# Optimization experiments

Measured on AMD Instinct MI355X. Metric: run time of the kernel, lower is better.

The kernel has to match this reference:

```python
import jax, jax.numpy as jnp
import numpy as np

L, B, T, V, E, H = 6, 4, 1024, 32000, 768, 12
D = E // H  # head_size = 64


def setup_inputs() -> dict:
    key = jax.random.key(0)
    ks = jax.random.split(key, 12)
    s = 0.02
    n = lambda k, shape: jax.random.normal(k, shape, jnp.float32) * s
    return {
        "idx": jax.random.randint(ks[0], (B, T), 0, V),
        "tok_emb": n(ks[1], (V, E)),
        "pos_emb": n(ks[2], (T, E)),
        "ln1_w": jnp.ones((L, E)), "ln1_b": jnp.zeros((L, E)),
        "wq": n(ks[3], (L, E, H, D)),
        "wk": n(ks[4], (L, E, H, D)),
        "wv": n(ks[5], (L, E, H, D)),
        "wo": n(ks[6], (L, E, E)), "bo": jnp.zeros((L, E)),
        "ln2_w": jnp.ones((L, E)), "ln2_b": jnp.zeros((L, E)),
        "w1": n(ks[7], (L, E, 4 * E)), "b1": jnp.zeros((L, 4 * E)),
        "w2": n(ks[8], (L, 4 * E, E)), "b2": jnp.zeros((L, E)),
        "lnf_w": jnp.ones((E,)), "lnf_b": jnp.zeros((E,)),
        "head_w": n(ks[9], (E, V)), "head_b": jnp.zeros((V,)),
    }


def _ln(x, w, b, eps=1e-5):
    m = x.mean(-1, keepdims=True)
    v = ((x - m) ** 2).mean(-1, keepdims=True)
    return (x - m) * jax.lax.rsqrt(v + eps) * w + b


def _forward(idx, tok_emb, pos_emb, ln1_w, ln1_b, wq, wk, wv, wo, bo,
             ln2_w, ln2_b, w1, b1, w2, b2, lnf_w, lnf_b, head_w, head_b):
    t = idx.shape[1]
    x = tok_emb[idx] + pos_emb[None, :t]          # [B,T,E]
    causal = jnp.tril(jnp.ones((t, t), bool))     # tril buffer
    scale = jnp.asarray(D, x.dtype) ** -0.5       # k.shape[-1] ** -0.5

    def block(x, p):
        l1w, l1b, Wq, Wk, Wv, Wo, Bo, l2w, l2b, W1, B1, W2, B2 = p
        h = _ln(x, l1w, l1b)
        q = jnp.einsum('btc,chd->bthd', h, Wq)
        k = jnp.einsum('btc,chd->bthd', h, Wk)
        v = jnp.einsum('btc,chd->bthd', h, Wv)
        wei = jnp.einsum('bqhd,bkhd->bhqk', q, k) * scale
        wei = jnp.where(causal, wei, -jnp.inf)
        wei = jax.nn.softmax(wei, axis=-1)
        att = jnp.einsum('bhqk,bkhd->bqhd', wei, v).reshape(x.shape)
        x = x + (att @ Wo + Bo)
        h2 = _ln(x, l2w, l2b)
        x = x + (jax.nn.relu(h2 @ W1 + B1) @ W2 + B2)
        return x, None

    params = (ln1_w, ln1_b, wq, wk, wv, wo, bo, ln2_w, ln2_b, w1, b1, w2, b2)
    x, _ = jax.lax.scan(block, x, params)
    x = _ln(x, lnf_w, lnf_b)
    return x @ head_w + head_b                    # [B,T,V] logits


def reference(idx, tok_emb, pos_emb, ln1_w, ln1_b, wq, wk, wv, wo, bo,
              ln2_w, ln2_b, w1, b1, w2, b2, lnf_w, lnf_b, head_w, head_b):
    return _forward(idx, tok_emb, pos_emb, ln1_w, ln1_b, wq, wk, wv, wo, bo,
                    ln2_w, ln2_b, w1, b1, w2, b2, lnf_w, lnf_b, head_w, head_b)
```

## Files before the change

kernel.cpp:

```cpp
#include <hip/hip_runtime.h>
#include <hip/hip_bf16.h>
#include <math.h>

#define L_LAYERS 6
#define BB 4
#define TT 1024
#define VV 32000
#define EE 768
#define HH 12
#define DD 64
#define BT (BB * TT)

typedef unsigned short u16;
typedef unsigned int   u32;
typedef __attribute__((ext_vector_type(8))) short short8;
typedef __attribute__((ext_vector_type(8))) unsigned short ushort8v;
typedef __attribute__((ext_vector_type(4))) unsigned short ushort4v;
typedef __attribute__((ext_vector_type(4))) float f32x4;

__device__ __forceinline__ float b2f_lo(u32 u) { union { u32 i; float f; } c; c.i = u << 16;          return c.f; }
__device__ __forceinline__ float b2f_hi(u32 u) { union { u32 i; float f; } c; c.i = u & 0xffff0000u;  return c.f; }
__device__ __forceinline__ u16  f2b(float f)   { union { float f; u32 i; } c{f}; u32 r = c.i + 0x7fffu + ((c.i >> 16) & 1u); return (u16)(r >> 16); }

__device__ __forceinline__ void gload16(const void* g, void* l) {
    __builtin_amdgcn_global_load_lds(
        (const __attribute__((address_space(1))) void*)g,
        (__attribute__((address_space(3))) void*)l, 16, 0, 0);
}

__global__ __launch_bounds__(256) void embed_kernel(
    const int* __restrict__ idx, const float* __restrict__ tok_emb,
    const float* __restrict__ pos_emb, float* __restrict__ x)
{
    int i = blockIdx.x * 256 + threadIdx.x;
    int e  = i % EE;
    int bt = i / EE;
    int t  = bt % TT;
    int tok = idx[bt];
    x[i] = tok_emb[(size_t)tok * EE + e] + pos_emb[(size_t)t * EE + e];
}

__global__ __launch_bounds__(256) void ln_kernel(
    const float* __restrict__ X, const float* __restrict__ w,
    const float* __restrict__ b, u16* __restrict__ Y)
{
    const int lane = threadIdx.x & 63;
    const size_t row = blockIdx.x * 4 + (threadIdx.x >> 6);
    const float* x = X + row * EE;

    f32x4 v[3];
    #pragma unroll
    for (int k = 0; k < 3; k++)
        v[k] = *(const f32x4*)&x[lane * 4 + k * 256];

    float s = 0.0f;
    #pragma unroll
    for (int k = 0; k < 3; k++) s += v[k][0] + v[k][1] + v[k][2] + v[k][3];
    #pragma unroll
    for (int off = 32; off; off >>= 1) s += __shfl_xor(s, off);
    const float mean = s * (1.0f / EE);

    float q = 0.0f;
    #pragma unroll
    for (int k = 0; k < 3; k++)
        #pragma unroll
        for (int j = 0; j < 4; j++) {
            v[k][j] -= mean;
            q += v[k][j] * v[k][j];
        }
    #pragma unroll
    for (int off = 32; off; off >>= 1) q += __shfl_xor(q, off);
    const float rstd = rsqrtf(q * (1.0f / EE) + 1e-5f);

    u16* y = Y + row * EE;
    #pragma unroll
    for (int k = 0; k < 3; k++) {
        const f32x4 wv = *(const f32x4*)&w[lane * 4 + k * 256];
        const f32x4 bv = *(const f32x4*)&b[lane * 4 + k * 256];
        ushort4v o;
        #pragma unroll
        for (int j = 0; j < 4; j++) o[j] = f2b(v[k][j] * rstd * wv[j] + bv[j]);
        *(ushort4v*)&y[lane * 4 + k * 256] = o;
    }
}

__device__ __forceinline__ void transpose_tile(
    const float* __restrict__ W, u16* __restrict__ Wt,
    int K, int N, int kt, int nt)
{
    __shared__ float t[32][33];
    const int k0 = kt * 32;
    const int n0 = nt * 32;
    const int c = threadIdx.x & 31;
    const int r = threadIdx.x >> 5;
    #pragma unroll
    for (int i = 0; i < 4; i++)
        t[r + i * 8][c] = W[(size_t)(k0 + r + i * 8) * N + n0 + c];
    __syncthreads();
    #pragma unroll
    for (int i = 0; i < 4; i++) {
        int rr = r + i * 8;
        Wt[(size_t)(n0 + rr) * K + k0 + c] = f2b(t[c][rr]);
    }
}

__global__ __launch_bounds__(256) void transpose_cvt(
    const float* __restrict__ W, u16* __restrict__ Wt, int K, int N)
{
    transpose_tile(W, Wt, K, N, blockIdx.y, blockIdx.x);
}

__global__ __launch_bounds__(256) void transpose_layer(
    const float* __restrict__ wq, const float* __restrict__ wk,
    const float* __restrict__ wv, const float* __restrict__ wo,
    const float* __restrict__ w1, const float* __restrict__ w2,
    u16* __restrict__ wt)
{
    const int t = blockIdx.x;
    if (t < 2304) {
        const int m = t / 576, r = t % 576;
        const float* Ws[4] = {wq, wk, wv, wo};
        transpose_tile(Ws[m], wt + (size_t)m * 768 * 768, 768, 768, r / 24, r % 24);
    } else if (t < 4608) {
        const int r = t - 2304;
        transpose_tile(w1, wt + (size_t)4 * 768 * 768, 768, 3072, r / 96, r % 96);
    } else {
        const int r = t - 4608;
        transpose_tile(w2, wt + (size_t)4 * 768 * 768 + (size_t)3072 * 768,
                       3072, 768, r / 24, r % 24);
    }
}

template<int RELU, int RES, int OUTBF, int MFRAG>
__global__ __launch_bounds__(256) void gemm_bf16(
    const u16* __restrict__ A, const u16* __restrict__ Bt,
    const float* __restrict__ bias, const float* __restrict__ res,
    void* __restrict__ Cv, int M, int N, int K)
{
    constexpr int TM = MFRAG * 32;
    __shared__ u16 As[TM * 64];
    __shared__ u16 Bs[128 * 64];

    const int tid  = threadIdx.x;
    const int lane = tid & 63;
    const int w    = tid >> 6;
    const int wr   = w >> 1, wc = w & 1;

    const int gx  = gridDim.x;
    const int nwg = gx * gridDim.y;
    const int lin = blockIdx.y * gx + blockIdx.x;
    const int q8  = nwg >> 3;
    const int s   = (lin & 7) * q8 + (lin >> 3);
    const int m0  = (s % gx) * TM;
    const int n0  = (s / gx) * 128;

    const int cs = (lane & 7) ^ (lane >> 3);
    const int rl = lane >> 3;

    int aoff[2 * MFRAG], boff[8];
    const int kq = lane >> 4;
    #pragma unroll
    for (int mi = 0; mi < MFRAG; mi++) {
        int rg = wr * (MFRAG * 16) + mi * 16 + (lane & 15);
        #pragma unroll
        for (int ks = 0; ks < 2; ks++)
            aoff[2 * mi + ks] = rg * 64 + (((ks * 4 + kq) ^ (rg & 7)) * 8);
    }
    #pragma unroll
    for (int ni = 0; ni < 4; ni++) {
        int rg = wc * 64 + ni * 16 + (lane & 15);
        #pragma unroll
        for (int ks = 0; ks < 2; ks++)
            boff[2 * ni + ks] = rg * 64 + (((ks * 4 + kq) ^ (rg & 7)) * 8);
    }

    f32x4 acc[MFRAG][4] = {};

    for (int k0 = 0; k0 < K; k0 += 64) {
        __syncthreads();
        #pragma unroll
        for (int i = 0; i < MFRAG; i++) {
            const int seg = i * 4 + w;
            const int row = seg * 8 + rl;
            gload16(A + (size_t)(m0 + row) * K + k0 + cs * 8, &As[seg * 512]);
        }
        #pragma unroll
        for (int i = 0; i < 4; i++) {
            const int seg = i * 4 + w;
            const int row = seg * 8 + rl;
            gload16(Bt + (size_t)(n0 + row) * K + k0 + cs * 8, &Bs[seg * 512]);
        }
        __syncthreads();
        #pragma unroll
        for (int ks = 0; ks < 2; ks++) {
            short8 af[MFRAG], bfv[4];
            #pragma unroll
            for (int mi = 0; mi < MFRAG; mi++) af[mi] = *(const short8*)&As[aoff[2 * mi + ks]];
            #pragma unroll
            for (int ni = 0; ni < 4; ni++) bfv[ni] = *(const short8*)&Bs[boff[2 * ni + ks]];
            #pragma unroll
            for (int mi = 0; mi < MFRAG; mi++)
                #pragma unroll
                for (int ni = 0; ni < 4; ni++)
                    acc[mi][ni] = __builtin_amdgcn_mfma_f32_16x16x32_bf16(
                        af[mi], bfv[ni], acc[mi][ni], 0, 0, 0);
        }
    }

    const int rbase = m0 + wr * (MFRAG * 16) + (lane >> 4) * 4;
    const int cbase = n0 + wc * 64 + (lane & 15);
    #pragma unroll
    for (int ni = 0; ni < 4; ni++) {
        const int c = cbase + ni * 16;
        const float bv = bias ? bias[c] : 0.0f;
        #pragma unroll
        for (int mi = 0; mi < MFRAG; mi++) {
            const int r = rbase + mi * 16;
            #pragma unroll
            for (int i = 0; i < 4; i++) {
                float v = acc[mi][ni][i] + bv;
                const size_t off = (size_t)(r + i) * N + c;
                if (RES)  v += res[off];
                if (RELU) v = fmaxf(v, 0.0f);
                if (OUTBF) ((u16*)Cv)[off] = f2b(v);
                else       ((float*)Cv)[off] = v;
            }
        }
    }
}

#define AST 72
__global__ __launch_bounds__(256) void attn_mfma(
    const u16* __restrict__ qkv, u16* __restrict__ O)
{
    const int tid = threadIdx.x;
    const int qi = blockIdx.x;
    const int h  = blockIdx.y;
    const int b  = blockIdx.z;
    const int q0 = qi * 64;

    __shared__ u16 Ks[2][64 * 64];
    __shared__ u16 Vt[2][64 * AST];
    __shared__ u16 Ps[64 * AST];

    const int lane = tid & 63;
    const int w    = tid >> 6;
    const int lr   = lane & 15;
    const int lk   = lane >> 4;

    const int cs = (lane & 7) ^ (lane >> 3);
    const int rl = lane >> 3;
    const int vk2 = tid & 31;
    const int vdc = tid >> 5;

    {
        const int sr = tid >> 2, sc = tid & 3;
        const u16* src = qkv + (size_t)(b * TT + q0 + sr) * 2304 + h * 64 + sc * 16;
        *(ushort8v*)&Ps[sr * AST + sc * 16]     = *(const ushort8v*)src;
        *(ushort8v*)&Ps[sr * AST + sc * 16 + 8] = *(const ushort8v*)(src + 8);
    }
    __syncthreads();
    short8 aq[2];
    #pragma unroll
    for (int ks = 0; ks < 2; ks++)
        aq[ks] = *(const short8*)&Ps[(w * 16 + lr) * AST + lk * 8 + ks * 32];

    ushort8v vr0, vr1;
    auto K_ISSUE = [&](int t, int bf) {
        const int k0 = t * 64;
        #pragma unroll
        for (int j = 0; j < 2; ++j) {
            const int seg = j * 4 + w;
            const int row = seg * 8 + rl;
            gload16(qkv + (size_t)(b * TT + k0 + row) * 2304 + 768 + h * 64 + cs * 8,
                    &Ks[bf][seg * 512]);
        }
    };
    auto V_LOAD = [&](int t) {
        const int k0 = t * 64;
        const u16* p = qkv + (size_t)(b * TT + k0 + 2 * vk2) * 2304 + 1536 + h * 64 + vdc * 8;
        vr0 = *(const ushort8v*)p;
        vr1 = *(const ushort8v*)(p + 2304);
    };
    auto V_WRITE = [&](int bf) {
        #pragma unroll
        for (int j = 0; j < 8; ++j) {
            const u32 val = (u32)vr0[j] | ((u32)vr1[j] << 16);
            *(u32*)&Vt[bf][(vdc * 8 + j) * AST + 2 * vk2] = val;
        }
    };

    K_ISSUE(0, 0);
    V_LOAD(0);
    V_WRITE(0);
    __syncthreads();

    f32x4 oacc[4] = {};
    float m_run[4], l_run[4];
    #pragma unroll
    for (int i = 0; i < 4; i++) { m_run[i] = -3.0e38f; l_run[i] = 0.0f; }

    const int qrow = q0 + w * 16 + lk * 4;
    const float SC = 0.18033688f;

    for (int t = 0; t <= qi; ++t) {
        const int cur = t & 1;

        f32x4 sfrag[4] = {};
        #pragma unroll
        for (int ks = 0; ks < 2; ks++)
            #pragma unroll
            for (int nt = 0; nt < 4; nt++) {
                const int rg = nt * 16 + lr;
                short8 bk = *(const short8*)&Ks[cur][rg * 64 + (((ks * 4 + lk) ^ (rg & 7)) * 8)];
                sfrag[nt] = __builtin_amdgcn_mfma_f32_16x16x32_bf16(aq[ks], bk, sfrag[nt], 0, 0, 0);
            }

        if (t < qi) { K_ISSUE(t + 1, cur ^ 1); V_LOAD(t + 1); }

        const int k0 = t * 64;
        float sv[4][4], mxv[4];
        float need = 0.0f;
        #pragma unroll
        for (int i = 0; i < 4; i++) {
            float mx = -3.0e38f;
            #pragma unroll
            for (int nt = 0; nt < 4; nt++) {
                float s = sfrag[nt][i] * SC;
                if (t == qi && (k0 + nt * 16 + lr) > (qrow + i)) s = -3.0e38f;
                sv[i][nt] = s;
                mx = fmaxf(mx, s);
            }
            mx = fmaxf(mx, __shfl_xor(mx, 1));
            mx = fmaxf(mx, __shfl_xor(mx, 2));
            mx = fmaxf(mx, __shfl_xor(mx, 4));
            mx = fmaxf(mx, __shfl_xor(mx, 8));
            mxv[i] = mx;
            need = fmaxf(need, mx - m_run[i]);
        }
        if (!__all(need <= 11.5f)) {
            #pragma unroll
            for (int i = 0; i < 4; i++) {
                const float m_new = fmaxf(m_run[i], mxv[i]);
                const float scale = exp2f(m_run[i] - m_new);
                l_run[i] *= scale;
                #pragma unroll
                for (int dt = 0; dt < 4; dt++) oacc[dt][i] *= scale;
                m_run[i] = m_new;
            }
        }
        #pragma unroll
        for (int i = 0; i < 4; i++) {
            float rs = 0.0f;
            #pragma unroll
            for (int nt = 0; nt < 4; nt++) {
                const float p = exp2f(sv[i][nt] - m_run[i]);
                sv[i][nt] = p;
                rs += p;
            }
            rs += __shfl_xor(rs, 1);
            rs += __shfl_xor(rs, 2);
            rs += __shfl_xor(rs, 4);
            rs += __shfl_xor(rs, 8);
            l_run[i] += rs;
        }

        #pragma unroll
        for (int i = 0; i < 4; i++)
            #pragma unroll
            for (int nt = 0; nt < 4; nt++)
                Ps[(w * 16 + lk * 4 + i) * AST + nt * 16 + lr] = f2b(sv[i][nt]);

        #pragma unroll
        for (int ks = 0; ks < 2; ks++) {
            short8 ap = *(const short8*)&Ps[(w * 16 + lr) * AST + lk * 8 + ks * 32];
            #pragma unroll
            for (int dt = 0; dt < 4; dt++) {
                short8 bv = *(const short8*)&Vt[cur][(dt * 16 + lr) * AST + lk * 8 + ks * 32];
                oacc[dt] = __builtin_amdgcn_mfma_f32_16x16x32_bf16(ap, bv, oacc[dt], 0, 0, 0);
            }
        }

        if (t < qi) V_WRITE(cur ^ 1);
        __syncthreads();
    }

    #pragma unroll
    for (int i = 0; i < 4; i++) {
        const float inv = 1.0f / l_run[i];
        u16* dst = O + (size_t)(b * TT + q0 + w * 16 + lk * 4 + i) * 768 + h * 64 + lr;
        #pragma unroll
        for (int dt = 0; dt < 4; dt++)
            dst[dt * 16] = f2b(oacc[dt][i] * inv);
    }
}

extern "C" void kernel_launch(void* const* d_in, const int* in_sizes, int n_in,
                              void* d_out, int out_size, void* d_ws, size_t ws_size,
                              hipStream_t stream)
{
    (void)in_sizes; (void)n_in; (void)out_size; (void)ws_size;

    const int*   idx     = (const int*)  d_in[0];
    const float* tok_emb = (const float*)d_in[1];
    const float* pos_emb = (const float*)d_in[2];
    const float* ln1_w   = (const float*)d_in[3];
    const float* ln1_b   = (const float*)d_in[4];
    const float* wq      = (const float*)d_in[5];
    const float* wk      = (const float*)d_in[6];
    const float* wv      = (const float*)d_in[7];
    const float* wo      = (const float*)d_in[8];
    const float* bo      = (const float*)d_in[9];
    const float* ln2_w   = (const float*)d_in[10];
    const float* ln2_b   = (const float*)d_in[11];
    const float* w1      = (const float*)d_in[12];
    const float* b1      = (const float*)d_in[13];
    const float* w2      = (const float*)d_in[14];
    const float* b2      = (const float*)d_in[15];
    const float* lnf_w   = (const float*)d_in[16];
    const float* lnf_b   = (const float*)d_in[17];
    const float* head_w  = (const float*)d_in[18];
    const float* head_b  = (const float*)d_in[19];
    float* out = (float*)d_out;

    const size_t S = (size_t)BT * EE;
    float* x   = (float*)d_ws;
    u16*  qkv  = (u16*)(x + S);
    u16*  hb   = qkv + (size_t)BT * 2304;
    u16*  ffh  = hb + S;
    u16*  wt   = ffh + (size_t)BT * 3072;

    embed_kernel<<<BT * EE / 256, 256, 0, stream>>>(idx, tok_emb, pos_emb, x);

    for (int l = 0; l < L_LAYERS; l++) {
        const size_t oE  = (size_t)l * EE;
        const size_t oEE = (size_t)l * EE * EE;
        const size_t oEF = (size_t)l * EE * 4 * EE;

        transpose_layer<<<6912, 256, 0, stream>>>(
            wq + oEE, wk + oEE, wv + oEE, wo + oEE, w1 + oEF, w2 + oEF, wt);

        ln_kernel<<<BT / 4, 256, 0, stream>>>(x, ln1_w + oE, ln1_b + oE, hb);
        gemm_bf16<0, 0, 1, 4><<<dim3(BT / 128, 2304 / 128), 256, 0, stream>>>(
            hb, wt, nullptr, nullptr, qkv, BT, 2304, 768);
        attn_mfma<<<dim3(TT / 64, HH, BB), 256, 0, stream>>>(qkv, hb);
        gemm_bf16<0, 1, 0, 2><<<dim3(BT / 64, 768 / 128), 256, 0, stream>>>(
            hb, wt + (size_t)3 * 768 * 768, bo + oE, x, x, BT, 768, 768);
        ln_kernel<<<BT / 4, 256, 0, stream>>>(x, ln2_w + oE, ln2_b + oE, hb);
        gemm_bf16<1, 0, 1, 4><<<dim3(BT / 128, 3072 / 128), 256, 0, stream>>>(
            hb, wt + (size_t)4 * 768 * 768, b1 + (size_t)l * 4 * EE, nullptr, ffh, BT, 3072, 768);
        gemm_bf16<0, 1, 0, 2><<<dim3(BT / 64, 768 / 128), 256, 0, stream>>>(
            ffh, wt + (size_t)4 * 768 * 768 + (size_t)3072 * 768, b2 + oE, x, x, BT, 768, 3072);
    }

    ln_kernel<<<BT / 4, 256, 0, stream>>>(x, lnf_w, lnf_b, hb);
    transpose_cvt<<<dim3(VV / 32, EE / 32), 256, 0, stream>>>(head_w, wt, EE, VV);
    gemm_bf16<0, 0, 0, 4><<<dim3(BT / 128, VV / 128), 256, 0, stream>>>(
        hb, wt, head_b, nullptr, out, BT, VV, 768);
}
```

Measured before the change: 1.555 ms.

## Enlarge attention query tile to 128 rows with 8 waves; drop GEMM tile swizzle

The attention kernel now processes 128 query rows per block with 512 threads, so each K/V tile loaded into shared memory serves twice as many queries. Waves whose rows lie entirely before a key tile skip its compute, and the causal mask is applied only on diagonal tiles. This cuts global K/V traffic per query and halves the number of blocks, at the cost of fewer, larger blocks and some idle waves near the diagonal. Separately, the GEMM drops its block-index swizzle and uses a plain row/column mapping, which may change L2 locality.

```diff
diff --git a/kernel.cpp b/kernel.cpp
--- a/kernel.cpp
+++ b/kernel.cpp
@@ -145,14 +145,8 @@
     const int lane = tid & 63;
     const int w    = tid >> 6;
     const int wr   = w >> 1, wc = w & 1;
-
-    const int gx  = gridDim.x;
-    const int nwg = gx * gridDim.y;
-    const int lin = blockIdx.y * gx + blockIdx.x;
-    const int q8  = nwg >> 3;
-    const int s   = (lin & 7) * q8 + (lin >> 3);
-    const int m0  = (s % gx) * TM;
-    const int n0  = (s / gx) * 128;
+    const int m0 = blockIdx.x * TM;
+    const int n0 = blockIdx.y * 128;
 
     const int cs = (lane & 7) ^ (lane >> 3);
     const int rl = lane >> 3;
@@ -230,18 +224,18 @@
 }
 
 #define AST 72
-__global__ __launch_bounds__(256) void attn_mfma(
+__global__ __launch_bounds__(512) void attn_mfma(
     const u16* __restrict__ qkv, u16* __restrict__ O)
 {
     const int tid = threadIdx.x;
     const int qi = blockIdx.x;
     const int h  = blockIdx.y;
     const int b  = blockIdx.z;
-    const int q0 = qi * 64;
+    const int q0 = qi * 128;
 
     __shared__ u16 Ks[2][64 * 64];
     __shared__ u16 Vt[2][64 * AST];
-    __shared__ u16 Ps[64 * AST];
+    __shared__ u16 Ps[128 * AST];
 
     const int lane = tid & 63;
     const int w    = tid >> 6;
@@ -251,7 +245,7 @@
     const int cs = (lane & 7) ^ (lane >> 3);
     const int rl = lane >> 3;
     const int vk2 = tid & 31;
-    const int vdc = tid >> 5;
+    const int vdc = (tid >> 5) & 15;
 
     {
         const int sr = tid >> 2, sc = tid & 3;
@@ -265,28 +259,24 @@
     for (int ks = 0; ks < 2; ks++)
         aq[ks] = *(const short8*)&Ps[(w * 16 + lr) * AST + lk * 8 + ks * 32];
 
-    ushort8v vr0, vr1;
+    ushort4v vr0, vr1;
     auto K_ISSUE = [&](int t, int bf) {
         const int k0 = t * 64;
-        #pragma unroll
-        for (int j = 0; j < 2; ++j) {
-            const int seg = j * 4 + w;
-            const int row = seg * 8 + rl;
-            gload16(qkv + (size_t)(b * TT + k0 + row) * 2304 + 768 + h * 64 + cs * 8,
-                    &Ks[bf][seg * 512]);
-        }
+        const int row = w * 8 + rl;
+        gload16(qkv + (size_t)(b * TT + k0 + row) * 2304 + 768 + h * 64 + cs * 8,
+                &Ks[bf][w * 512]);
     };
     auto V_LOAD = [&](int t) {
         const int k0 = t * 64;
-        const u16* p = qkv + (size_t)(b * TT + k0 + 2 * vk2) * 2304 + 1536 + h * 64 + vdc * 8;
-        vr0 = *(const ushort8v*)p;
-        vr1 = *(const ushort8v*)(p + 2304);
+        const u16* p = qkv + (size_t)(b * TT + k0 + 2 * vk2) * 2304 + 1536 + h * 64 + vdc * 4;
+        vr0 = *(const ushort4v*)p;
+        vr1 = *(const ushort4v*)(p + 2304);
     };
     auto V_WRITE = [&](int bf) {
         #pragma unroll
-        for (int j = 0; j < 8; ++j) {
+        for (int j = 0; j < 4; ++j) {
             const u32 val = (u32)vr0[j] | ((u32)vr1[j] << 16);
-            *(u32*)&Vt[bf][(vdc * 8 + j) * AST + 2 * vk2] = val;
+            *(u32*)&Vt[bf][(vdc * 4 + j) * AST + 2 * vk2] = val;
         }
     };
 
@@ -301,87 +291,95 @@
     for (int i = 0; i < 4; i++) { m_run[i] = -3.0e38f; l_run[i] = 0.0f; }
 
     const int qrow = q0 + w * 16 + lk * 4;
+    const int wmax = q0 + w * 16 + 15;
+    const int ntile = 2 * qi + 2;
     const float SC = 0.18033688f;
 
-    for (int t = 0; t <= qi; ++t) {
+    for (int t = 0; t < ntile; ++t) {
         const int cur = t & 1;
+        const int k0 = t * 64;
+        const bool active = (k0 <= wmax);
 
         f32x4 sfrag[4] = {};
-        #pragma unroll
-        for (int ks = 0; ks < 2; ks++)
-            #pragma unroll
-            for (int nt = 0; nt < 4; nt++) {
-                const int rg = nt * 16 + lr;
-                short8 bk = *(const short8*)&Ks[cur][rg * 64 + (((ks * 4 + lk) ^ (rg & 7)) * 8)];
-                sfrag[nt] = __builtin_amdgcn_mfma_f32_16x16x32_bf16(aq[ks], bk, sfrag[nt], 0, 0, 0);
+        if (active) {
+            #pragma unroll
+            for (int ks = 0; ks < 2; ks++)
+                #pragma unroll
+                for (int nt = 0; nt < 4; nt++) {
+                    const int rg = nt * 16 + lr;
+                    short8 bk = *(const short8*)&Ks[cur][rg * 64 + (((ks * 4 + lk) ^ (rg & 7)) * 8)];
+                    sfrag[nt] = __builtin_amdgcn_mfma_f32_16x16x32_bf16(aq[ks], bk, sfrag[nt], 0, 0, 0);
+                }
+        }
+
+        if (t + 1 < ntile) { K_ISSUE(t + 1, cur ^ 1); V_LOAD(t + 1); }
+
+        if (active) {
+            const bool diag = (k0 + 63 > qrow);
+            float sv[4][4], mxv[4];
+            float need = 0.0f;
+            #pragma unroll
+            for (int i = 0; i < 4; i++) {
+                float mx = -3.0e38f;
+                #pragma unroll
+                for (int nt = 0; nt < 4; nt++) {
+                    float s = sfrag[nt][i] * SC;
+                    if (diag && (k0 + nt * 16 + lr) > (qrow + i)) s = -3.0e38f;
+                    sv[i][nt] = s;
+                    mx = fmaxf(mx, s);
+                }
+                mx = fmaxf(mx, __shfl_xor(mx, 1));
+                mx = fmaxf(mx, __shfl_xor(mx, 2));
+                mx = fmaxf(mx, __shfl_xor(mx, 4));
+                mx = fmaxf(mx, __shfl_xor(mx, 8));
+                mxv[i] = mx;
+                need = fmaxf(need, mx - m_run[i]);
             }
-
-        if (t < qi) { K_ISSUE(t + 1, cur ^ 1); V_LOAD(t + 1); }
-
-        const int k0 = t * 64;
-        float sv[4][4], mxv[4];
-        float need = 0.0f;
-        #pragma unroll
-        for (int i = 0; i < 4; i++) {
-            float mx = -3.0e38f;
-            #pragma unroll
-            for (int nt = 0; nt < 4; nt++) {
-                float s = sfrag[nt][i] * SC;
-                if (t == qi && (k0 + nt * 16 + lr) > (qrow + i)) s = -3.0e38f;
-                sv[i][nt] = s;
-                mx = fmaxf(mx, s);
+            if (!__all(need <= 11.5f)) {
+                #pragma unroll
+                for (int i = 0; i < 4; i++) {
+                    const float m_new = fmaxf(m_run[i], mxv[i]);
+                    const float scale = exp2f(m_run[i] - m_new);
+                    l_run[i] *= scale;
+                    #pragma unroll
+                    for (int dt = 0; dt < 4; dt++) oacc[dt][i] *= scale;
+                    m_run[i] = m_new;
+                }
             }
-            mx = fmaxf(mx, __shfl_xor(mx, 1));
-            mx = fmaxf(mx, __shfl_xor(mx, 2));
-            mx = fmaxf(mx, __shfl_xor(mx, 4));
-            mx = fmaxf(mx, __shfl_xor(mx, 8));
-            mxv[i] = mx;
-            need = fmaxf(need, mx - m_run[i]);
-        }
-        if (!__all(need <= 11.5f)) {
             #pragma unroll
             for (int i = 0; i < 4; i++) {
-                const float m_new = fmaxf(m_run[i], mxv[i]);
-                const float scale = exp2f(m_run[i] - m_new);
-                l_run[i] *= scale;
-                #pragma unroll
-                for (int dt = 0; dt < 4; dt++) oacc[dt][i] *= scale;
-                m_run[i] = m_new;
+                float rs = 0.0f;
+                #pragma unroll
+                for (int nt = 0; nt < 4; nt++) {
+                    const float p = exp2f(sv[i][nt] - m_run[i]);
+                    sv[i][nt] = p;
+                    rs += p;
+                }
+                rs += __shfl_xor(rs, 1);
+                rs += __shfl_xor(rs, 2);
+                rs += __shfl_xor(rs, 4);
+                rs += __shfl_xor(rs, 8);
+                l_run[i] += rs;
             }
-        }
-        #pragma unroll
-        for (int i = 0; i < 4; i++) {
-            float rs = 0.0f;
-            #pragma unroll
-            for (int nt = 0; nt < 4; nt++) {
-                const float p = exp2f(sv[i][nt] - m_run[i]);
-                sv[i][nt] = p;
-                rs += p;
+
+            #pragma unroll
+            for (int i = 0; i < 4; i++)
+                #pragma unroll
+                for (int nt = 0; nt < 4; nt++)
+                    Ps[(w * 16 + lk * 4 + i) * AST + nt * 16 + lr] = f2b(sv[i][nt]);
+
+            #pragma unroll
+            for (int ks = 0; ks < 2; ks++) {
+                short8 ap = *(const short8*)&Ps[(w * 16 + lr) * AST + lk * 8 + ks * 32];
+                #pragma unroll
+                for (int dt = 0; dt < 4; dt++) {
+                    short8 bv = *(const short8*)&Vt[cur][(dt * 16 + lr) * AST + lk * 8 + ks * 32];
+                    oacc[dt] = __builtin_amdgcn_mfma_f32_16x16x32_bf16(ap, bv, oacc[dt], 0, 0, 0);
+                }
             }
-            rs += __shfl_xor(rs, 1);
-            rs += __shfl_xor(rs, 2);
-            rs += __shfl_xor(rs, 4);
-            rs += __shfl_xor(rs, 8);
-            l_run[i] += rs;
-        }
-
-        #pragma unroll
-        for (int i = 0; i < 4; i++)
-            #pragma unroll
-            for (int nt = 0; nt < 4; nt++)
-                Ps[(w * 16 + lk * 4 + i) * AST + nt * 16 + lr] = f2b(sv[i][nt]);
-
-        #pragma unroll
-        for (int ks = 0; ks < 2; ks++) {
-            short8 ap = *(const short8*)&Ps[(w * 16 + lr) * AST + lk * 8 + ks * 32];
-            #pragma unroll
-            for (int dt = 0; dt < 4; dt++) {
-                short8 bv = *(const short8*)&Vt[cur][(dt * 16 + lr) * AST + lk * 8 + ks * 32];
-                oacc[dt] = __builtin_amdgcn_mfma_f32_16x16x32_bf16(ap, bv, oacc[dt], 0, 0, 0);
-            }
-        }
-
-        if (t < qi) V_WRITE(cur ^ 1);
+        }
+
+        if (t + 1 < ntile) V_WRITE(cur ^ 1);
         __syncthreads();
     }
 
@@ -443,7 +441,7 @@
         ln_kernel<<<BT / 4, 256, 0, stream>>>(x, ln1_w + oE, ln1_b + oE, hb);
         gemm_bf16<0, 0, 1, 4><<<dim3(BT / 128, 2304 / 128), 256, 0, stream>>>(
             hb, wt, nullptr, nullptr, qkv, BT, 2304, 768);
-        attn_mfma<<<dim3(TT / 64, HH, BB), 256, 0, stream>>>(qkv, hb);
+        attn_mfma<<<dim3(TT / 128, HH, BB), 512, 0, stream>>>(qkv, hb);
         gemm_bf16<0, 1, 0, 2><<<dim3(BT / 64, 768 / 128), 256, 0, stream>>>(
             hb, wt + (size_t)3 * 768 * 768, bo + oE, x, x, BT, 768, 768);
         ln_kernel<<<BT / 4, 256, 0, stream>>>(x, ln2_w + oE, ln2_b + oE, hb);
```

Measured after the change: 1.529 ms. No clear change (-1.7%).

## Compute softmax row sums via extra MFMA ones column; drop GEMM tile swizzle

Applied to the files above, without the earlier changes.

The attention kernel appends a 16-row block to the transposed V tile whose first row is bf16 1.0, so a fifth MFMA per k-step accumulates the softmax denominator, replacing the per-row exp sum and four cross-lane shuffles. The final normalizer is read with a shuffle from the extra accumulator. Because the sum now uses the bf16-rounded probabilities, numerics shift slightly, and shared memory and registers grow. Separately, the GEMM kernel drops its XCD-aware block remapping and uses plain blockIdx tiling, which may change L2 locality.

```diff
diff --git a/kernel.cpp b/kernel.cpp
--- a/kernel.cpp
+++ b/kernel.cpp
@@ -145,14 +145,8 @@
     const int lane = tid & 63;
     const int w    = tid >> 6;
     const int wr   = w >> 1, wc = w & 1;
-
-    const int gx  = gridDim.x;
-    const int nwg = gx * gridDim.y;
-    const int lin = blockIdx.y * gx + blockIdx.x;
-    const int q8  = nwg >> 3;
-    const int s   = (lin & 7) * q8 + (lin >> 3);
-    const int m0  = (s % gx) * TM;
-    const int n0  = (s / gx) * 128;
+    const int m0 = blockIdx.x * TM;
+    const int n0 = blockIdx.y * 128;
 
     const int cs = (lane & 7) ^ (lane >> 3);
     const int rl = lane >> 3;
@@ -240,7 +234,7 @@
     const int q0 = qi * 64;
 
     __shared__ u16 Ks[2][64 * 64];
-    __shared__ u16 Vt[2][64 * AST];
+    __shared__ u16 Vt[2][80 * AST];
     __shared__ u16 Ps[64 * AST];
 
     const int lane = tid & 63;
@@ -252,6 +246,13 @@
     const int rl = lane >> 3;
     const int vk2 = tid & 31;
     const int vdc = tid >> 5;
+
+    for (int i = tid; i < 16 * AST; i += 256) {
+        const int r = i / AST, c = i % AST;
+        const u16 v = (r == 0) ? (u16)0x3F80 : (u16)0;
+        Vt[0][(64 + r) * AST + c] = v;
+        Vt[1][(64 + r) * AST + c] = v;
+    }
 
     {
         const int sr = tid >> 2, sc = tid & 3;
@@ -295,10 +296,10 @@
     V_WRITE(0);
     __syncthreads();
 
-    f32x4 oacc[4] = {};
-    float m_run[4], l_run[4];
-    #pragma unroll
-    for (int i = 0; i < 4; i++) { m_run[i] = -3.0e38f; l_run[i] = 0.0f; }
+    f32x4 oacc[5] = {};
+    float m_run[4];
+    #pragma unroll
+    for (int i = 0; i < 4; i++) m_run[i] = -3.0e38f;
 
     const int qrow = q0 + w * 16 + lk * 4;
     const float SC = 0.18033688f;
@@ -343,27 +344,16 @@
             for (int i = 0; i < 4; i++) {
                 const float m_new = fmaxf(m_run[i], mxv[i]);
                 const float scale = exp2f(m_run[i] - m_new);
-                l_run[i] *= scale;
                 #pragma unroll
-                for (int dt = 0; dt < 4; dt++) oacc[dt][i] *= scale;
+                for (int dt = 0; dt < 5; dt++) oacc[dt][i] *= scale;
                 m_run[i] = m_new;
             }
         }
         #pragma unroll
-        for (int i = 0; i < 4; i++) {
-            float rs = 0.0f;
-            #pragma unroll
-            for (int nt = 0; nt < 4; nt++) {
-                const float p = exp2f(sv[i][nt] - m_run[i]);
-                sv[i][nt] = p;
-                rs += p;
-            }
-            rs += __shfl_xor(rs, 1);
-            rs += __shfl_xor(rs, 2);
-            rs += __shfl_xor(rs, 4);
-            rs += __shfl_xor(rs, 8);
-            l_run[i] += rs;
-        }
+        for (int i = 0; i < 4; i++)
+            #pragma unroll
+            for (int nt = 0; nt < 4; nt++)
+                sv[i][nt] = exp2f(sv[i][nt] - m_run[i]);
 
         #pragma unroll
         for (int i = 0; i < 4; i++)
@@ -375,7 +365,7 @@
         for (int ks = 0; ks < 2; ks++) {
             short8 ap = *(const short8*)&Ps[(w * 16 + lr) * AST + lk * 8 + ks * 32];
             #pragma unroll
-            for (int dt = 0; dt < 4; dt++) {
+            for (int dt = 0; dt < 5; dt++) {
                 short8 bv = *(const short8*)&Vt[cur][(dt * 16 + lr) * AST + lk * 8 + ks * 32];
                 oacc[dt] = __builtin_amdgcn_mfma_f32_16x16x32_bf16(ap, bv, oacc[dt], 0, 0, 0);
             }
@@ -387,7 +377,8 @@
 
     #pragma unroll
     for (int i = 0; i < 4; i++) {
-        const float inv = 1.0f / l_run[i];
+        const float li  = __shfl(oacc[4][i], lane & 48);
+        const float inv = 1.0f / li;
         u16* dst = O + (size_t)(b * TT + q0 + w * 16 + lk * 4 + i) * 768 + h * 64 + lr;
         #pragma unroll
         for (int dt = 0; dt < 4; dt++)
```

Result: faster. 1.425 ms (-8.4%).
